# Kernel tuning notes

Hardware: AMD Instinct MI355X
Metric: run time of the kernel (lower is better)

## Reference

```python
import math
import jax, jax.numpy as jnp
import numpy as np

B, A, M, NC = 32, 8400, 32, 80
TOP_K, ALPHA, BETA, EPS = 13, 1.0, 6.0, 1e-9
IMG = 640.0


def _ciou(b1, b2, eps=1e-7):
    # b1, b2 broadcastable [..., 4]; CIoU as in compute_iou (box1=gt, box2=pred)
    b1x1, b1y1, b1x2, b1y2 = b1[..., 0], b1[..., 1], b1[..., 2], b1[..., 3]
    b2x1, b2y1, b2x2, b2y2 = b2[..., 0], b2[..., 1], b2[..., 2], b2[..., 3]
    w1, h1 = b1x2 - b1x1, b1y2 - b1y1 + eps
    w2, h2 = b2x2 - b2x1, b2y2 - b2y1 + eps
    inter = (jnp.minimum(b1x2, b2x2) - jnp.maximum(b1x1, b2x1)).clip(0) * \
            (jnp.minimum(b1y2, b2y2) - jnp.maximum(b1y1, b2y1)).clip(0)
    union = w1 * h1 + w2 * h2 - inter + eps
    iou = inter / union
    cw = jnp.maximum(b1x2, b2x2) - jnp.minimum(b1x1, b2x1)
    ch = jnp.maximum(b1y2, b2y2) - jnp.minimum(b1y1, b2y1)
    c2 = cw ** 2 + ch ** 2 + eps
    rho2 = ((b2x1 + b2x2 - b1x1 - b1x2) ** 2 + (b2y1 + b2y2 - b1y1 - b1y2) ** 2) / 4.0
    v = (4.0 / math.pi ** 2) * (jnp.arctan(w2 / h2) - jnp.arctan(w1 / h1)) ** 2
    alpha = jax.lax.stop_gradient(v / (v - iou + (1.0 + eps)))
    return iou - (rho2 / c2 + v * alpha)


def setup_inputs() -> dict:
    key = jax.random.key(0)
    ks = jax.random.split(key, 8)
    pd_scores = jax.random.uniform(ks[0], (B, A, NC), jnp.float32)
    anc_points = jax.random.uniform(ks[1], (A, 2), jnp.float32) * IMG
    # predicted boxes around anchor points (valid x1<x2, y1<y2)
    off = jax.random.uniform(ks[2], (B, A, 4), jnp.float32) * 80.0 + 2.0
    pd_bboxes = jnp.concatenate([anc_points[None] - off[..., :2],
                                 anc_points[None] + off[..., 2:]], -1)
    # GT boxes: random centers and sizes, clipped to image
    c = jax.random.uniform(ks[3], (B, M, 2), jnp.float32) * IMG
    wh = jax.random.uniform(ks[4], (B, M, 2), jnp.float32) * 180.0 + 20.0
    gt_bboxes = jnp.concatenate([(c - wh / 2).clip(0, IMG), (c + wh / 2).clip(0, IMG)], -1)
    gt_labels = jax.random.randint(ks[5], (B, M, 1), 0, NC, jnp.int64)
    n_valid = jax.random.randint(ks[6], (B,), 1, M + 1)
    mask_gt = (jnp.arange(M)[None, :] < n_valid[:, None]).astype(jnp.float32)[..., None]
    return {"pd_scores": pd_scores, "pd_bboxes": pd_bboxes, "anc_points": anc_points,
            "gt_labels": gt_labels, "gt_bboxes": gt_bboxes, "mask_gt": mask_gt}


def reference(pd_scores, pd_bboxes, anc_points, gt_labels, gt_bboxes, mask_gt):
    b, a, nc = pd_scores.shape
    m = gt_bboxes.shape[1]
    dtype = pd_scores.dtype

    # anchors-inside-GT mask: [B,M,A]
    lt = gt_bboxes[:, :, None, :2]          # [B,M,1,2]
    rb = gt_bboxes[:, :, None, 2:]
    deltas = jnp.concatenate([anc_points[None, None] - lt,
                              rb - anc_points[None, None]], -1)  # [B,M,A,4]
    mask_in_gts = deltas.min(-1) > EPS
    mg = mask_gt[..., 0] > 0                 # [B,M] bool
    gt_mask = mask_in_gts & mg[:, :, None]

    # per-GT class score gather: pd_scores[b, :, gt_labels[b,m]] -> [B,M,A]
    labels = gt_labels[..., 0]               # [B,M]
    idx = jnp.broadcast_to(labels[:, :, None, None], (b, m, a, 1))
    gathered = jnp.take_along_axis(jnp.broadcast_to(pd_scores[:, None], (b, m, a, nc)), idx, axis=3)[..., 0]
    bbox_scores = jnp.where(gt_mask, gathered, 0.0)

    # CIoU overlaps (dense, masked) [B,M,A]
    iou = _ciou(gt_bboxes[:, :, None, :], pd_bboxes[:, None, :, :])
    overlaps = jnp.where(gt_mask, jnp.maximum(iou, 0.0), 0.0)

    align_metric = bbox_scores ** ALPHA * overlaps ** BETA

    # top-k selection with duplicate suppression (faithful to scatter_add loop)
    _, tk_idx = jax.lax.top_k(align_metric, TOP_K)      # [B,M,K]
    tk_mask = jnp.broadcast_to(mg[:, :, None], tk_idx.shape)
    tk_idx = jnp.where(tk_mask, tk_idx, 0)
    bi = jnp.arange(b)[:, None, None]
    mi = jnp.arange(m)[None, :, None]
    counts = jnp.zeros((b, m, a), jnp.int32).at[bi, mi, tk_idx].add(1)
    mask_top_k = jnp.where(counts > 1, 0, counts).astype(dtype)

    mask_pos = mask_top_k * mask_in_gts.astype(dtype) * mg[:, :, None].astype(dtype)
    fg_mask = mask_pos.sum(1)                            # [B,A]

    # resolve anchors assigned to multiple GTs (no-op when none; matches torch branch)
    mask_multi = fg_mask[:, None, :] > 1                 # [B,M,A] (broadcast)
    max_idx = overlaps.argmax(1)                         # [B,A]
    is_max = (jnp.arange(m)[None, :, None] == max_idx[:, None, :]).astype(dtype)
    mask_pos = jnp.where(mask_multi, is_max, mask_pos)
    fg_mask = mask_pos.sum(1)

    target_gt_idx = mask_pos.argmax(1)                   # [B,A]
    target_labels = jnp.maximum(jnp.take_along_axis(labels, target_gt_idx, axis=1), 0)
    target_bboxes = jnp.take_along_axis(
        gt_bboxes, jnp.broadcast_to(target_gt_idx[..., None], (b, a, 4)), axis=1)

    target_scores = jax.nn.one_hot(target_labels, NC, dtype=dtype)
    target_scores = jnp.where((fg_mask > 0)[..., None], target_scores, 0.0)

    am = align_metric * mask_pos
    pos_am = am.max(-1, keepdims=True)                   # [B,M,1]
    pos_ov = (overlaps * mask_pos).max(-1, keepdims=True)
    norm = (am * pos_ov / (pos_am + EPS)).max(1)[..., None]  # [B,A,1]
    target_scores = target_scores * norm

    return target_bboxes, target_scores, fg_mask > 0
```

## Files before the change

kernel.cpp:

```cpp
#include <hip/hip_runtime.h>
#include <math.h>

#define BB 32
#define AA 8400
#define MM 32
#define NCC 80
#define TOPK 13
#define CAP 1024
#define NW (AA / 32 + 1)
#define T12 512

typedef float nfloat4 __attribute__((ext_vector_type(4)));

__device__ __forceinline__ void wave_argmax(float& v, int& i) {
    #pragma unroll
    for (int off = 32; off > 0; off >>= 1) {
        float ov = __shfl_xor(v, off, 64);
        int oi = __shfl_xor(i, off, 64);
        if (ov > v || (ov == v && oi < i)) { v = ov; i = oi; }
    }
}

__global__ __launch_bounds__(T12, 8) void k12_topk(
        const float* __restrict__ pd_scores, const float* __restrict__ pd_bboxes,
        const float* __restrict__ anc, const int* __restrict__ gt_labels,
        const float* __restrict__ gt_bboxes, const float* __restrict__ mask_gt,
        int* __restrict__ sel_idx, float* __restrict__ sel_ov, float* __restrict__ sel_am,
        float* __restrict__ pos_am, float* __restrict__ pos_ov) {
    __shared__ float lval[CAP];
    __shared__ int   lidx[CAP];
    __shared__ float oval[CAP];
    __shared__ unsigned int bmask[NW];
    __shared__ float lw[8][TOPK];
    __shared__ int   li[8][TOPK];
    __shared__ float lo[8][TOPK];
    __shared__ int   wsum[8];
    __shared__ int   s_p, s_sel;
    const float eps = 1e-7f;
    int bx = blockIdx.x;
    int jj = bx >> 3;
    int b  = (bx & 7) * 4 + (jj >> 5);
    int m  = jj & 31;
    int bm = b * MM + m;
    int tid = threadIdx.x;
    int lane = tid & 63;
    int wid = tid >> 6;
    if (tid == 0) pos_am[bm] = 0.f;
    if (tid == 1) pos_ov[bm] = 0.f;
    if (tid == 2) s_p = 0;
    if (tid == 3) s_sel = 0;
    if (tid < 16) sel_idx[bm * 16 + tid] = -1;
    if (!(mask_gt[bm] > 0.f)) return;

    for (int i = tid; i < NW; i += T12) bmask[i] = 0u;
    float4 g = reinterpret_cast<const float4*>(gt_bboxes)[bm];

    const float4* anc4 = reinterpret_cast<const float4*>(anc);
    unsigned long long bits = 0ull;
    int c_t = 0;
    #pragma unroll
    for (int j = 0; j < 9; j++) {
        int e = tid + (j << 9);
        if (e < 4200) {
            float4 an = anc4[e];
            float d0 = fminf(fminf(an.x - g.x, an.y - g.y), fminf(g.z - an.x, g.w - an.y));
            float d1 = fminf(fminf(an.z - g.x, an.w - g.y), fminf(g.z - an.z, g.w - an.w));
            if (d0 > 1e-9f) { bits |= 1ull << (2 * j);     c_t++; }
            if (d1 > 1e-9f) { bits |= 1ull << (2 * j + 1); c_t++; }
        }
    }
    int x = c_t;
    #pragma unroll
    for (int off = 1; off < 64; off <<= 1) {
        int y = __shfl_up(x, off, 64);
        if (lane >= off) x += y;
    }
    if (lane == 63) wsum[wid] = x;
    __syncthreads();
    int base = 0;
    #pragma unroll
    for (int w = 0; w < 8; w++) if (w < wid) base += wsum[w];
    int n_c = 0;
    #pragma unroll
    for (int w = 0; w < 8; w++) n_c += wsum[w];
    n_c = min(n_c, CAP);
    {
        int o = base + x - c_t;
        unsigned long long mm_ = bits;
        while (mm_) {
            int k = __builtin_ctzll(mm_);
            mm_ &= mm_ - 1ull;
            int i = 2 * tid + 1024 * (k >> 1) + (k & 1);
            if (o < CAP) lidx[o] = i;
            o++;
        }
    }
    for (int s = n_c + tid; s < CAP; s += T12) { lval[s] = -1.f; lidx[s] = AA; }
    __syncthreads();

    float w1 = g.z - g.x, h1 = g.w - g.y + eps;
    float atg = atanf(w1 / h1);
    float w1h1 = w1 * h1;
    float sgx = g.x + g.z, sgy = g.y + g.w;
    int lab = gt_labels[bm];
    const float4* pbb = reinterpret_cast<const float4*>(pd_bboxes) + (long)b * AA;
    const float* scp = pd_scores + (long)b * AA * NCC + lab;
    float rv0 = -1.f, rv1 = -1.f;
    float rov0 = 0.f, rov1 = 0.f;
    int   ri0 = AA,   ri1 = AA;
    {
        int    ci0, ci1;
        float4 pb0, pb1;
        float  sc0, sc1;
        ci0 = (tid < n_c)        ? lidx[tid]        : -1;
        ci1 = (tid + T12 < n_c)  ? lidx[tid + T12]  : -1;
        if (ci0 >= 0) { pb0 = pbb[ci0]; sc0 = scp[(long)ci0 * NCC]; ri0 = ci0; }
        if (ci1 >= 0) { pb1 = pbb[ci1]; sc1 = scp[(long)ci1 * NCC]; ri1 = ci1; }
        int pcnt = 0;
        #define CIOU_SLOT(CI, PB, SC, RV, ROV, S)                                     \
            if (CI >= 0) {                                                            \
                float w2 = PB.z - PB.x, h2 = PB.w - PB.y + eps;                       \
                float iw = fmaxf(fminf(g.z, PB.z) - fmaxf(g.x, PB.x), 0.f);           \
                float ih = fmaxf(fminf(g.w, PB.w) - fmaxf(g.y, PB.y), 0.f);           \
                float inter = iw * ih;                                                \
                float uni = w1h1 + w2 * h2 - inter + eps;                             \
                float iou = inter / uni;                                              \
                float cw = fmaxf(g.z, PB.z) - fminf(g.x, PB.x);                       \
                float ch = fmaxf(g.w, PB.w) - fminf(g.y, PB.y);                       \
                float c2 = cw * cw + ch * ch + eps;                                   \
                float dx = PB.x + PB.z - sgx, dy = PB.y + PB.w - sgy;                 \
                float rho2 = (dx * dx + dy * dy) * 0.25f;                             \
                float dv = atanf(w2 / h2) - atg;                                      \
                float v = 0.4052847345693511f * dv * dv;                              \
                float alpha = v / (v - iou + (1.0f + eps));                           \
                float cv = iou - (rho2 / c2 + v * alpha);                             \
                float ov = fmaxf(cv, 0.f);                                            \
                float o2 = ov * ov;                                                   \
                float val = SC * o2 * o2 * o2;                   \
                bool pos = val > 0.f;                                                 \
                RV = pos ? val : -1.f;                                                \
                ROV = ov;                                                             \
                lval[S] = RV;                                                         \
                oval[S] = ov;                                                         \
                if (pos) { atomicOr(&bmask[CI >> 5], 1u << (CI & 31)); pcnt++; }      \
            }
        CIOU_SLOT(ci0, pb0, sc0, rv0, rov0, tid)
        CIOU_SLOT(ci1, pb1, sc1, rv1, rov1, tid + T12)
        #undef CIOU_SLOT
        #pragma unroll
        for (int off = 32; off > 0; off >>= 1) pcnt += __shfl_xor(pcnt, off, 64);
        if (lane == 0) atomicAdd(&s_p, pcnt);
    }
    __syncthreads();
    int p = s_p;

    if (p >= TOPK) {
        for (int k = 0; k < TOPK; k++) {
            float bv = rv0; int bi = ri0;
            if (rv1 > bv || (rv1 == bv && ri1 < bi)) { bv = rv1; bi = ri1; }
            wave_argmax(bv, bi);
            if (ri0 == bi && bi < AA) { rv0 = -1.f; lo[wid][k] = rov0; }
            if (ri1 == bi && bi < AA) { rv1 = -1.f; lo[wid][k] = rov1; }
            if (lane == 0) { lw[wid][k] = bv; li[wid][k] = bi; }
        }
        __syncthreads();
        if (wid == 0) {
            float mv0 = -1.f, mv1 = -1.f, mo0 = 0.f, mo1 = 0.f;
            int mi0 = AA, mi1 = AA;
            int e0 = 2 * lane, e1 = 2 * lane + 1;
            if (e0 < 8 * TOPK) {
                int w = e0 / TOPK, k = e0 - w * TOPK;
                mv0 = lw[w][k]; mi0 = li[w][k]; mo0 = lo[w][k];
            }
            if (e1 < 8 * TOPK) {
                int w = e1 / TOPK, k = e1 - w * TOPK;
                mv1 = lw[w][k]; mi1 = li[w][k]; mo1 = lo[w][k];
            }
            for (int k = 0; k < TOPK; k++) {
                float bv = mv0; int bi = mi0;
                if (mv1 > bv || (mv1 == bv && mi1 < bi)) { bv = mv1; bi = mi1; }
                wave_argmax(bv, bi);
                if (mi0 == bi && mv0 > -1.f) {
                    sel_idx[bm * 16 + k] = bi;
                    sel_am[bm * 16 + k] = mv0;
                    sel_ov[bm * 16 + k] = mo0;
                    mv0 = -1.f;
                } else if (mi1 == bi && mv1 > -1.f) {
                    sel_idx[bm * 16 + k] = bi;
                    sel_am[bm * 16 + k] = mv1;
                    sel_ov[bm * 16 + k] = mo1;
                    mv1 = -1.f;
                }
            }
        }
    } else {
        for (int s = tid; s < n_c; s += T12)
            if (lval[s] > 0.f) {
                int slot = atomicAdd(&s_sel, 1);
                sel_idx[bm * 16 + slot] = lidx[s];
                sel_ov[bm * 16 + slot] = oval[s];
                sel_am[bm * 16 + slot] = lval[s];
            }
        if (wid == 0) {
            int need = TOPK - p;
            for (int base_i = 0; need > 0 && base_i < AA; base_i += 64) {
                int i = base_i + lane;
                bool cand = (i < AA) && !((bmask[i >> 5] >> (i & 31)) & 1u);
                unsigned long long wm = __ballot(cand);
                int take = min(need, (int)__popcll(wm));
                if (cand && (int)__popcll(wm & ((1ull << lane) - 1ull)) < take) {
                    float2 an = reinterpret_cast<const float2*>(anc)[i];
                    float dmin = fminf(fminf(an.x - g.x, an.y - g.y), fminf(g.z - an.x, g.w - an.y));
                    if (dmin > 1e-9f) {
                        float4 pb = pbb[i];
                        float w2 = pb.z - pb.x, h2 = pb.w - pb.y + eps;
                        float iw = fmaxf(fminf(g.z, pb.z) - fmaxf(g.x, pb.x), 0.f);
                        float ih = fmaxf(fminf(g.w, pb.w) - fmaxf(g.y, pb.y), 0.f);
                        float inter = iw * ih;
                        float uni = w1h1 + w2 * h2 - inter + eps;
                        float iou = inter / uni;
                        float cw = fmaxf(g.z, pb.z) - fminf(g.x, pb.x);
                        float ch = fmaxf(g.w, pb.w) - fminf(g.y, pb.y);
                        float c2 = cw * cw + ch * ch + eps;
                        float dx = pb.x + pb.z - sgx, dy = pb.y + pb.w - sgy;
                        float rho2 = (dx * dx + dy * dy) * 0.25f;
                        float dv = atanf(w2 / h2) - atg;
                        float v = 0.4052847345693511f * dv * dv;
                        float alpha = v / (v - iou + (1.0f + eps));
                        float ov = fmaxf(iou - (rho2 / c2 + v * alpha), 0.f);
                        int slot = atomicAdd(&s_sel, 1);
                        sel_idx[bm * 16 + slot] = i;
                        sel_ov[bm * 16 + slot] = ov;
                        sel_am[bm * 16 + slot] = 0.f;
                    }
                }
                need -= take;
            }
        }
    }
}

__global__ __launch_bounds__(256) void k3_resolve(
        const float* __restrict__ pd_scores, const float* __restrict__ pd_bboxes,
        const float* __restrict__ anc, const int* __restrict__ gt_labels,
        const float* __restrict__ gt_bboxes, const float* __restrict__ mask_gt,
        const int* __restrict__ sel_idx, const float* __restrict__ sel_ov,
        const float* __restrict__ sel_am,
        float* __restrict__ pos_am, float* __restrict__ pos_ov,
        float* __restrict__ out_bbox, float* __restrict__ out_fg,
        int2* __restrict__ meta) {
    __shared__ float sg[MM][8];
    __shared__ int slab[MM];
    __shared__ int smg[MM];
    __shared__ unsigned int selcol[256];
    __shared__ float sov[256];
    __shared__ float sam[256];
    const float eps = 1e-7f;
    int b = blockIdx.y;
    int tid = threadIdx.x;
    if (tid < MM) {
        int gm = b * MM + tid;
        float4 g = reinterpret_cast<const float4*>(gt_bboxes)[gm];
        float w1 = g.z - g.x, h1 = g.w - g.y + eps;
        sg[tid][0] = g.x; sg[tid][1] = g.y; sg[tid][2] = g.z; sg[tid][3] = g.w;
        sg[tid][4] = w1 * h1;
        sg[tid][5] = atanf(w1 / h1);
        sg[tid][6] = g.x + g.z;
        sg[tid][7] = g.y + g.w;
        int lb = gt_labels[gm]; if (lb < 0) lb = 0;
        slab[tid] = lb;
        smg[tid] = mask_gt[gm] > 0.f ? 1 : 0;
    }
    selcol[tid] = 0u;
    __syncthreads();
    int a0 = blockIdx.x * 256;
    const int* sl = sel_idx + b * MM * 16;
    #pragma unroll
    for (int t = tid; t < MM * 16; t += 256) {
        int e = sl[t];
        if (e >= a0 && e < a0 + 256) {
            atomicOr(&selcol[e - a0], 1u << (t >> 4));
            sov[e - a0] = sel_ov[b * MM * 16 + t];
            sam[e - a0] = sel_am[b * MM * 16 + t];
        }
    }
    __syncthreads();
    int a = a0 + tid;
    if (a >= AA) return;
    int g = b * AA + a;
    unsigned int sel = selcol[tid];
    int fg = __popc(sel);

    int tg = 0; bool fgo = false; float ovt = 0.f; float amv = 0.f;
    if (fg == 1) {
        tg = __ffs(sel) - 1;
        ovt = sov[tid];
        amv = sam[tid];
        fgo = true;
    } else if (fg > 1) {
        float ax = anc[a * 2], ay = anc[a * 2 + 1];
        float4 pb = reinterpret_cast<const float4*>(pd_bboxes)[g];
        float w2 = pb.z - pb.x, h2 = pb.w - pb.y + eps;
        float atp = atanf(w2 / h2);
        float w2h2 = w2 * h2;
        float spx = pb.x + pb.z, spy = pb.y + pb.w;
        float bestov = -1.f; int bestm = 0;
        for (int mm = 0; mm < MM; mm++) {
            float gx1 = sg[mm][0], gy1 = sg[mm][1], gx2 = sg[mm][2], gy2 = sg[mm][3];
            float dmin = fminf(fminf(ax - gx1, ay - gy1), fminf(gx2 - ax, gy2 - ay));
            float ov = 0.f;
            if ((dmin > 1e-9f) && smg[mm]) {
                float iw = fmaxf(fminf(gx2, pb.z) - fmaxf(gx1, pb.x), 0.f);
                float ih = fmaxf(fminf(gy2, pb.w) - fmaxf(gy1, pb.y), 0.f);
                float inter = iw * ih;
                float uni = sg[mm][4] + w2h2 - inter + eps;
                float iou = inter / uni;
                float cw = fmaxf(gx2, pb.z) - fminf(gx1, pb.x);
                float ch = fmaxf(gy2, pb.w) - fminf(gy1, pb.y);
                float c2 = cw * cw + ch * ch + eps;
                float dx = spx - sg[mm][6], dy = spy - sg[mm][7];
                float rho2 = (dx * dx + dy * dy) * 0.25f;
                float dv = atp - sg[mm][5];
                float v = 0.4052847345693511f * dv * dv;
                float alpha = v / (v - iou + (1.0f + eps));
                ov = fmaxf(iou - (rho2 / c2 + v * alpha), 0.f);
            }
            if (ov > bestov) { bestov = ov; bestm = mm; }
        }
        tg = bestm; ovt = bestov;
        float sc = pd_scores[(long)g * NCC + slab[tg]];
        float o2 = ovt * ovt;
        amv = sc * o2 * o2 * o2;
        fgo = true;
    }

    nfloat4 gb = {sg[tg][0], sg[tg][1], sg[tg][2], sg[tg][3]};
    __builtin_nontemporal_store(gb, reinterpret_cast<nfloat4*>(out_bbox) + g);
    out_fg[g] = fgo ? 1.f : 0.f;
    if (fgo) {
        atomicMax((int*)&pos_am[b * MM + tg], __float_as_int(amv));
        atomicMax((int*)&pos_ov[b * MM + tg], __float_as_int(ovt));
    }
    meta[g] = make_int2(__float_as_int(amv), tg | (slab[tg] << 8) | ((fgo ? 1 : 0) << 16));
}

__global__ __launch_bounds__(256) void k4_scores(
        const int2* __restrict__ meta,
        const float* __restrict__ pos_am, const float* __restrict__ pos_ov,
        float* __restrict__ out_scores) {
    int g = blockIdx.x * 256 + threadIdx.x;
    const int NQ = NCC / 4;
    if (g >= BB * AA * NQ) return;
    int ba = g / NQ;
    int c0 = (g % NQ) * 4;
    nfloat4 o = {0.f, 0.f, 0.f, 0.f};
    int2 mt = meta[ba];
    int p = mt.y;
    if (p & (1 << 16)) {
        int tg = p & 31, lab = (p >> 8) & 127;
        int b = ba / AA;
        int bm = b * MM + tg;
        float nv = (__int_as_float(mt.x) * pos_ov[bm]) / (pos_am[bm] + 1e-9f);
        int d = lab - c0;
        if (d == 0) o.x = nv; else if (d == 1) o.y = nv;
        else if (d == 2) o.z = nv; else if (d == 3) o.w = nv;
    }
    __builtin_nontemporal_store(o, reinterpret_cast<nfloat4*>(out_scores) + g);
}

extern "C" void kernel_launch(void* const* d_in, const int* in_sizes, int n_in,
                              void* d_out, int out_size, void* d_ws, size_t ws_size,
                              hipStream_t stream) {
    const float* pd_scores = (const float*)d_in[0];
    const float* pd_bboxes = (const float*)d_in[1];
    const float* anc       = (const float*)d_in[2];
    const int*   gt_labels = (const int*)d_in[3];
    const float* gt_bboxes = (const float*)d_in[4];
    const float* mask_gt   = (const float*)d_in[5];

    const long nBA = (long)BB * AA;

    char* ws = (char*)d_ws;
    int*   sel_idx = (int*)ws;                  ws += (long)BB * MM * 16 * 4;
    float* sel_ov  = (float*)ws;                ws += (long)BB * MM * 16 * 4;
    float* sel_am  = (float*)ws;                ws += (long)BB * MM * 16 * 4;
    float* pos_am  = (float*)ws;                ws += BB * MM * 4;
    float* pos_ov  = (float*)ws;                ws += BB * MM * 4;
    int2*  meta    = (int2*)ws;                 ws += nBA * 8;

    float* out_bbox   = (float*)d_out;
    float* out_scores = out_bbox + nBA * 4;
    float* out_fg     = out_scores + nBA * NCC;

    k12_topk<<<BB * MM, T12, 0, stream>>>(pd_scores, pd_bboxes, anc, gt_labels,
                                          gt_bboxes, mask_gt, sel_idx, sel_ov, sel_am,
                                          pos_am, pos_ov);
    dim3 g3((AA + 255) / 256, BB);
    k3_resolve<<<g3, 256, 0, stream>>>(pd_scores, pd_bboxes, anc, gt_labels,
                                       gt_bboxes, mask_gt, sel_idx, sel_ov, sel_am,
                                       pos_am, pos_ov, out_bbox, out_fg, meta);
    long nS4 = nBA * (NCC / 4);
    k4_scores<<<(int)((nS4 + 255) / 256), 256, 0, stream>>>(meta, pos_am, pos_ov, out_scores);
}
```

Before: 196.5 us.

## Zero score tensor in resolve kernel and scatter only foreground scores

The resolve kernel now writes zeros to its slice of the dense score output and appends each foreground anchor to a per-batch compact list via an atomic counter. A new small scatter kernel, one block per batch, fills in the normalized score for listed anchors only. This replaces the per-element dense scores pass and the per-anchor meta buffer. It also drops the block-index swizzle in the top-k kernel. The risk is list overflow if a batch has more than 512 foreground anchors, and a scatter grid of only 32 blocks.

```diff
diff --git a/kernel.cpp b/kernel.cpp
--- a/kernel.cpp
+++ b/kernel.cpp
@@ -9,6 +9,7 @@
 #define CAP 1024
 #define NW (AA / 32 + 1)
 #define T12 512
+#define FGCAP 512
 
 typedef float nfloat4 __attribute__((ext_vector_type(4)));
 
@@ -26,7 +27,8 @@
         const float* __restrict__ anc, const int* __restrict__ gt_labels,
         const float* __restrict__ gt_bboxes, const float* __restrict__ mask_gt,
         int* __restrict__ sel_idx, float* __restrict__ sel_ov, float* __restrict__ sel_am,
-        float* __restrict__ pos_am, float* __restrict__ pos_ov) {
+        float* __restrict__ pos_am, float* __restrict__ pos_ov,
+        int* __restrict__ fgcnt) {
     __shared__ float lval[CAP];
     __shared__ int   lidx[CAP];
     __shared__ float oval[CAP];
@@ -37,11 +39,9 @@
     __shared__ int   wsum[8];
     __shared__ int   s_p, s_sel;
     const float eps = 1e-7f;
-    int bx = blockIdx.x;
-    int jj = bx >> 3;
-    int b  = (bx & 7) * 4 + (jj >> 5);
-    int m  = jj & 31;
-    int bm = b * MM + m;
+    int bm = blockIdx.x;
+    int b = bm >> 5;
+    int m = bm & 31;
     int tid = threadIdx.x;
     int lane = tid & 63;
     int wid = tid >> 6;
@@ -49,6 +49,7 @@
     if (tid == 1) pos_ov[bm] = 0.f;
     if (tid == 2) s_p = 0;
     if (tid == 3) s_sel = 0;
+    if (m == 0 && tid == 4) fgcnt[b] = 0;
     if (tid < 16) sel_idx[bm * 16 + tid] = -1;
     if (!(mask_gt[bm] > 0.f)) return;
 
@@ -248,7 +249,8 @@
         const float* __restrict__ sel_am,
         float* __restrict__ pos_am, float* __restrict__ pos_ov,
         float* __restrict__ out_bbox, float* __restrict__ out_fg,
-        int2* __restrict__ meta) {
+        float* __restrict__ out_scores,
+        int* __restrict__ fgcnt, int2* __restrict__ fglist) {
     __shared__ float sg[MM][8];
     __shared__ int slab[MM];
     __shared__ int smg[MM];
@@ -285,6 +287,13 @@
         }
     }
     __syncthreads();
+    {
+        nfloat4 z = {0.f, 0.f, 0.f, 0.f};
+        nfloat4* outs4 = reinterpret_cast<nfloat4*>(out_scores) + ((long)b * AA + a0) * (NCC / 4);
+        int lim = (AA - a0 < 256 ? AA - a0 : 256) * (NCC / 4);
+        for (int idx = tid; idx < lim; idx += 256)
+            __builtin_nontemporal_store(z, outs4 + idx);
+    }
     int a = a0 + tid;
     if (a >= AA) return;
     int g = b * AA + a;
@@ -340,32 +349,26 @@
     if (fgo) {
         atomicMax((int*)&pos_am[b * MM + tg], __float_as_int(amv));
         atomicMax((int*)&pos_ov[b * MM + tg], __float_as_int(ovt));
-    }
-    meta[g] = make_int2(__float_as_int(amv), tg | (slab[tg] << 8) | ((fgo ? 1 : 0) << 16));
+        int slot = atomicAdd(&fgcnt[b], 1);
+        fglist[b * FGCAP + slot] = make_int2(a | (tg << 14) | (slab[tg] << 19), __float_as_int(amv));
+    }
 }
 
-__global__ __launch_bounds__(256) void k4_scores(
-        const int2* __restrict__ meta,
+__global__ __launch_bounds__(256) void k4_scatter(
+        const int* __restrict__ fgcnt, const int2* __restrict__ fglist,
         const float* __restrict__ pos_am, const float* __restrict__ pos_ov,
         float* __restrict__ out_scores) {
-    int g = blockIdx.x * 256 + threadIdx.x;
-    const int NQ = NCC / 4;
-    if (g >= BB * AA * NQ) return;
-    int ba = g / NQ;
-    int c0 = (g % NQ) * 4;
-    nfloat4 o = {0.f, 0.f, 0.f, 0.f};
-    int2 mt = meta[ba];
-    int p = mt.y;
-    if (p & (1 << 16)) {
-        int tg = p & 31, lab = (p >> 8) & 127;
-        int b = ba / AA;
-        int bm = b * MM + tg;
-        float nv = (__int_as_float(mt.x) * pos_ov[bm]) / (pos_am[bm] + 1e-9f);
-        int d = lab - c0;
-        if (d == 0) o.x = nv; else if (d == 1) o.y = nv;
-        else if (d == 2) o.z = nv; else if (d == 3) o.w = nv;
-    }
-    __builtin_nontemporal_store(o, reinterpret_cast<nfloat4*>(out_scores) + g);
+    int b = blockIdx.x;
+    int n = fgcnt[b];
+    for (int t = threadIdx.x; t < n; t += 256) {
+        int2 e = fglist[b * FGCAP + t];
+        int a   = e.x & 16383;
+        int tg  = (e.x >> 14) & 31;
+        int lab = (e.x >> 19) & 127;
+        int bmi = b * MM + tg;
+        float nv = (__int_as_float(e.y) * pos_ov[bmi]) / (pos_am[bmi] + 1e-9f);
+        out_scores[((long)b * AA + a) * NCC + lab] = nv;
+    }
 }
 
 extern "C" void kernel_launch(void* const* d_in, const int* in_sizes, int n_in,
@@ -386,7 +389,8 @@
     float* sel_am  = (float*)ws;                ws += (long)BB * MM * 16 * 4;
     float* pos_am  = (float*)ws;                ws += BB * MM * 4;
     float* pos_ov  = (float*)ws;                ws += BB * MM * 4;
-    int2*  meta    = (int2*)ws;                 ws += nBA * 8;
+    int*   fgcnt   = (int*)ws;                  ws += BB * 4;
+    int2*  fglist  = (int2*)ws;                 ws += (long)BB * FGCAP * 8;
 
     float* out_bbox   = (float*)d_out;
     float* out_scores = out_bbox + nBA * 4;
@@ -394,11 +398,11 @@
 
     k12_topk<<<BB * MM, T12, 0, stream>>>(pd_scores, pd_bboxes, anc, gt_labels,
                                           gt_bboxes, mask_gt, sel_idx, sel_ov, sel_am,
-                                          pos_am, pos_ov);
+                                          pos_am, pos_ov, fgcnt);
     dim3 g3((AA + 255) / 256, BB);
     k3_resolve<<<g3, 256, 0, stream>>>(pd_scores, pd_bboxes, anc, gt_labels,
                                        gt_bboxes, mask_gt, sel_idx, sel_ov, sel_am,
-                                       pos_am, pos_ov, out_bbox, out_fg, meta);
-    long nS4 = nBA * (NCC / 4);
-    k4_scores<<<(int)((nS4 + 255) / 256), 256, 0, stream>>>(meta, pos_am, pos_ov, out_scores);
+                                       pos_am, pos_ov, out_bbox, out_fg, out_scores,
+                                       fgcnt, fglist);
+    k4_scatter<<<BB, 256, 0, stream>>>(fgcnt, fglist, pos_am, pos_ov, out_scores);
 }
```

Measured after the change: 218.6 us. 11.2% more time.
